# Kernel tuning notes

Measured on AMD Instinct MI355X. Metric: run time of the kernel, lower is better.

## Reference

```python
import jax, jax.numpy as jnp
import numpy as np

HEIGHT = 16   # RoIRotate(height=16)
MAX_W = 128   # static padded width (== max achievable new_width given box generation)


def setup_inputs() -> dict:
    key = jax.random.key(0)
    k1, k2, k3, k4, k5 = jax.random.split(key, 5)
    B, C, H, W, N = 8, 32, 512, 512, 64
    image = jax.random.normal(k1, (B, C, H, W), dtype=jnp.float32)
    # Box geometry: heights in [8,40], aspect ratio in [1,8] -> new_width in [16,128]
    bh = jax.random.uniform(k2, (B, N), minval=8.0, maxval=40.0)
    ar = jax.random.uniform(k3, (B, N), minval=1.0, maxval=8.0)
    bw = bh * ar
    left = jax.random.uniform(k4, (B, N)) * (W - 1.0 - bw)
    top = jax.random.uniform(k5, (B, N)) * (H - 1.0 - bh)
    theta = jnp.zeros((B, N), dtype=jnp.float32)  # theta unused by the module
    boxes = jnp.stack([left, top, left + bw, top + bh, theta], axis=-1).astype(jnp.float32)
    return {"image": image, "boxes": boxes}


def _roi_rotate(image, boxes):
    B, C, H, W = image.shape
    left, top, right, bottom = boxes[..., 0], boxes[..., 1], boxes[..., 2], boxes[..., 3]
    bw = right - left                       # base_widths  [B,N]
    bh = bottom - top                       # base_heights [B,N]
    # aspect = bw/bh; NaN (0/0) -> width 0, as in the torch code
    aspect = jnp.where(bh > 0, bw / jnp.maximum(bh, 1e-6), 0.0)
    new_w = jnp.clip((aspect * HEIGHT).astype(jnp.int32), 0, MAX_W)  # [B,N]
    each_w = bw / jnp.maximum(new_w - 1, 1).astype(jnp.float32)
    each_h = bh / float(HEIGHT - 1)
    kx = jnp.arange(MAX_W, dtype=jnp.float32)
    ky = jnp.arange(HEIGHT, dtype=jnp.float32)
    xx = kx[None, None, :] * each_w[..., None] + left[..., None]   # [B,N,MAX_W]
    yy = ky[None, None, :] * each_h[..., None] + top[..., None]    # [B,N,HEIGHT]
    x0 = jnp.clip(jnp.floor(xx).astype(jnp.int32), 0, W - 1)
    x1 = jnpp_clip = jnp.clip(x0 + 1, 0, W - 1)
    y0 = jnp.clip(jnp.floor(yy).astype(jnp.int32), 0, H - 1)
    y1 = jnp.clip(y0 + 1, 0, H - 1)
    im_flat = image.reshape(B, C, H * W)

    def g(imf, ylin, xlin):
        # imf [C,H*W], ylin [N,Hh], xlin [N,Wm] -> [C,N,Hh,Wm]
        lin = ylin[:, :, None] * W + xlin[:, None, :]
        return imf[:, lin]

    gather = jax.vmap(g)
    Ia = gather(im_flat, y0, x0)  # [B,C,N,Hh,Wm]
    Ib = gather(im_flat, y1, x0)
    Ic = gather(im_flat, y0, x1)
    Id = gather(im_flat, y1, x1)
    # weights use the clamped corner coordinates, matching the torch code
    wx1 = x1.astype(jnp.float32) - xx       # [B,N,MAX_W]
    wx0 = xx - x0.astype(jnp.float32)
    wy1 = y1.astype(jnp.float32) - yy       # [B,N,HEIGHT]
    wy0 = yy - y0.astype(jnp.float32)
    WX1 = wx1[:, None, :, None, :]
    WX0 = wx0[:, None, :, None, :]
    WY1 = wy1[:, None, :, :, None]
    WY0 = wy0[:, None, :, :, None]
    res = Ia * WX1 * WY1 + Ib * WX1 * WY0 + Ic * WX0 * WY1 + Id * WX0 * WY0
    mask = jnp.arange(MAX_W)[None, None, :] < new_w[..., None]    # [B,N,MAX_W]
    res = res * mask[:, None, :, None, :].astype(res.dtype)
    res = jnp.transpose(res, (0, 2, 1, 3, 4))                      # [B,N,C,Hh,Wm]
    return res, mask.astype(jnp.uint8)


def reference(image, boxes):
    return _roi_rotate(image, boxes)
```

## Files before the change

kernel.cpp:

```cpp
#include <hip/hip_runtime.h>

#define BB 8
#define CC 32
#define HH 512
#define WW 512
#define NN 64
#define RH 16
#define RW 128

#define RES_ELEMS ((size_t)BB * NN * CC * RH * RW)

__global__ __launch_bounds__(256) void roi_fused(const float* __restrict__ img,
                                                 const float* __restrict__ boxes,
                                                 float* __restrict__ out,
                                                 float* __restrict__ mout) {
    const int tid = threadIdx.x;
    const int k   = tid & (RW - 1);
    const int jh  = tid >> 7;
    const unsigned blk = blockIdx.x;
    const int c   = blk & (CC - 1);
    const int bn  = blk >> 5;
    const int b   = bn >> 6;

    const float* bx = boxes + (size_t)bn * 5;
    const float left = bx[0];
    const float top  = bx[1];
    const float bw   = bx[2] - left;
    const float bh   = bx[3] - top;
    const float aspect = (bh > 0.0f) ? (bw / fmaxf(bh, 1e-6f)) : 0.0f;
    int new_w = (int)(aspect * (float)RH);
    new_w = min(max(new_w, 0), RW);
    const float each_w = bw / (float)max(new_w - 1, 1);
    const float each_h = bh / (float)(RH - 1);

    float* outp = out + (size_t)blk * (RH * RW) + (size_t)jh * (8 * RW) + k;

    if (c == 0 && jh == 0)
        mout[(size_t)bn * RW + k] = (k < new_w) ? 1.0f : 0.0f;

    if (k < new_w) {
        const float xx = (float)k * each_w + left;
        int x0 = (int)floorf(xx);
        x0 = min(max(x0, 0), WW - 1);
        const int x1  = min(x0 + 1, WW - 1);
        const int xg  = min(x0, WW - 2);
        const bool edge = (x0 == WW - 1);
        const float wx1 = (float)x1 - xx;
        const float wx0 = xx - (float)x0;

        const float* imf = img + ((size_t)(b * CC + c) * (HH * WW)) + xg;

        #pragma unroll
        for (int jj = 0; jj < 8; ++jj) {
            const int j = jh * 8 + jj;
            const float yy = (float)j * each_h + top;
            int y0 = (int)floorf(yy);
            y0 = min(max(y0, 0), HH - 1);
            const int y1 = min(y0 + 1, HH - 1);
            const float wy1 = (float)y1 - yy;
            const float wy0 = yy - (float)y0;

            const float* rowA = imf + (size_t)y0 * WW;
            const float* rowB = imf + (size_t)y1 * WW;
            const float a0 = rowA[0], a1 = rowA[1];
            const float b0 = rowB[0], b1 = rowB[1];
            const float Ia = edge ? a1 : a0;
            const float Ic = a1;
            const float Ib = edge ? b1 : b0;
            const float Id = b1;

            const float val = Ia * wx1 * wy1 + Ib * wx1 * wy0
                            + Ic * wx0 * wy1 + Id * wx0 * wy0;
            outp[(size_t)jj * RW] = val;
        }
    } else {
        #pragma unroll
        for (int jj = 0; jj < 8; ++jj)
            outp[(size_t)jj * RW] = 0.0f;
    }
}

extern "C" void kernel_launch(void* const* d_in, const int* in_sizes, int n_in,
                              void* d_out, int out_size, void* d_ws, size_t ws_size,
                              hipStream_t stream) {
    const float* img   = (const float*)d_in[0];
    const float* boxes = (const float*)d_in[1];
    float* out  = (float*)d_out;
    float* mout = out + RES_ELEMS;

    const int blocks = BB * NN * CC;
    roi_fused<<<blocks, 256, 0, stream>>>(img, boxes, out, mout);
}
```

Baseline: 379.4 us.

## Process eight channels per block reusing precomputed bilinear offsets and weights

```diff
diff --git a/kernel.cpp b/kernel.cpp
--- a/kernel.cpp
+++ b/kernel.cpp
@@ -7,8 +7,11 @@
 #define NN 64
 #define RH 16
 #define RW 128
+#define HWSZ (HH * WW)
 
 #define RES_ELEMS ((size_t)BB * NN * CC * RH * RW)
+
+struct __attribute__((aligned(4))) f2 { float x, y; };
 
 __global__ __launch_bounds__(256) void roi_fused(const float* __restrict__ img,
                                                  const float* __restrict__ boxes,
@@ -18,8 +21,8 @@
     const int k   = tid & (RW - 1);
     const int jh  = tid >> 7;
     const unsigned blk = blockIdx.x;
-    const int c   = blk & (CC - 1);
-    const int bn  = blk >> 5;
+    const int cg  = blk & 3;
+    const int bn  = blk >> 2;
     const int b   = bn >> 6;
 
     const float* bx = boxes + (size_t)bn * 5;
@@ -33,50 +36,52 @@
     const float each_w = bw / (float)max(new_w - 1, 1);
     const float each_h = bh / (float)(RH - 1);
 
-    float* outp = out + (size_t)blk * (RH * RW) + (size_t)jh * (8 * RW) + k;
-
-    if (c == 0 && jh == 0)
+    if (cg == 0 && jh == 0)
         mout[(size_t)bn * RW + k] = (k < new_w) ? 1.0f : 0.0f;
 
-    if (k < new_w) {
-        const float xx = (float)k * each_w + left;
-        int x0 = (int)floorf(xx);
-        x0 = min(max(x0, 0), WW - 1);
-        const int x1  = min(x0 + 1, WW - 1);
-        const int xg  = min(x0, WW - 2);
-        const bool edge = (x0 == WW - 1);
-        const float wx1 = (float)x1 - xx;
-        const float wx0 = xx - (float)x0;
+    const bool active = (k < new_w);
 
-        const float* imf = img + ((size_t)(b * CC + c) * (HH * WW)) + xg;
+    const float xx = (float)k * each_w + left;
+    int x0 = (int)floorf(xx);
+    x0 = min(max(x0, 0), WW - 1);
+    const int x1 = min(x0 + 1, WW - 1);
+    const int xg = min(x0, WW - 2);
+    float wx1 = (float)x1 - xx;
+    float wx0 = xx - (float)x0;
+    if (!active) { wx1 = 0.0f; wx0 = 0.0f; }
 
+    int   offA[8], offB[8];
+    float w00[8], w01[8], w10[8], w11[8];
+    #pragma unroll
+    for (int jj = 0; jj < 8; ++jj) {
+        const int j = jh * 8 + jj;
+        const float yy = (float)j * each_h + top;
+        int y0 = (int)floorf(yy);
+        y0 = min(max(y0, 0), HH - 1);
+        const int y1 = min(y0 + 1, HH - 1);
+        const float wy1 = (float)y1 - yy;
+        const float wy0 = yy - (float)y0;
+        offA[jj] = y0 * WW + xg;
+        offB[jj] = y1 * WW + xg;
+        w00[jj] = wx1 * wy1;
+        w10[jj] = wx0 * wy1;
+        w01[jj] = wx1 * wy0;
+        w11[jj] = wx0 * wy0;
+    }
+
+    const float* plane0 = img + (size_t)(b * CC + cg * 8) * HWSZ;
+    float* outp0 = out + (((size_t)bn * CC + cg * 8) * RH + (size_t)jh * 8) * RW + k;
+
+    for (int ci = 0; ci < 8; ++ci) {
+        const float* pl = plane0 + (size_t)ci * HWSZ;
+        float* op = outp0 + (size_t)ci * (RH * RW);
         #pragma unroll
         for (int jj = 0; jj < 8; ++jj) {
-            const int j = jh * 8 + jj;
-            const float yy = (float)j * each_h + top;
-            int y0 = (int)floorf(yy);
-            y0 = min(max(y0, 0), HH - 1);
-            const int y1 = min(y0 + 1, HH - 1);
-            const float wy1 = (float)y1 - yy;
-            const float wy0 = yy - (float)y0;
-
-            const float* rowA = imf + (size_t)y0 * WW;
-            const float* rowB = imf + (size_t)y1 * WW;
-            const float a0 = rowA[0], a1 = rowA[1];
-            const float b0 = rowB[0], b1 = rowB[1];
-            const float Ia = edge ? a1 : a0;
-            const float Ic = a1;
-            const float Ib = edge ? b1 : b0;
-            const float Id = b1;
-
-            const float val = Ia * wx1 * wy1 + Ib * wx1 * wy0
-                            + Ic * wx0 * wy1 + Id * wx0 * wy0;
-            outp[(size_t)jj * RW] = val;
+            const f2 A  = *(const f2*)(pl + offA[jj]);
+            const f2 Bv = *(const f2*)(pl + offB[jj]);
+            op[jj * RW] = A.x * w00[jj] + A.y * w10[jj]
+                        + Bv.x * w01[jj] + Bv.y * w11[jj];
         }
-    } else {
-        #pragma unroll
-        for (int jj = 0; jj < 8; ++jj)
-            outp[(size_t)jj * RW] = 0.0f;
     }
 }
 
@@ -88,6 +93,6 @@
     float* out  = (float*)d_out;
     float* mout = out + RES_ELEMS;
 
-    const int blocks = BB * NN * CC;
+    const int blocks = BB * NN * 4;
     roi_fused<<<blocks, 256, 0, stream>>>(img, boxes, out, mout);
 }
```

New measurement: 439.4 us. 1.16x slower.
